# Kernel tuning notes

Hardware: AMD Instinct MI355X
Metric: run time of the kernel (lower is better)

The kernel has to match this reference:

```python
import jax, jax.numpy as jnp
import numpy as np
import math

B, N, ND, ED, CD, H = 4, 128, 256, 128, 256, 8
D = ND // H

def _ln(x):
    m = jnp.mean(x, axis=-1, keepdims=True)
    v = jnp.mean((x - m) ** 2, axis=-1, keepdims=True)
    return (x - m) / jnp.sqrt(v + 1e-5)

def _lrelu(x):
    return jax.nn.leaky_relu(x, negative_slope=0.1)

def setup_inputs() -> dict:
    key = jax.random.key(0)
    ks = jax.random.split(key, 16)
    rn = lambda k, s: jax.random.normal(k, s, jnp.float32) * 0.02
    return {
        "nodes": jax.random.normal(ks[0], (B, N, ND), jnp.float32),
        "edges": jax.random.normal(ks[1], (B, N, N, ED), jnp.float32),
        "conds": jax.random.normal(ks[2], (B, 1, CD), jnp.float32),
        "Wc": rn(ks[3], (CD, 4 * ND)), "bc": jnp.zeros((4 * ND,), jnp.float32),
        "Wqkv": rn(ks[4], (ND, 3 * ND)), "bqkv": jnp.zeros((3 * ND,), jnp.float32),
        "Wss": rn(ks[5], (ED, 2 * ND)), "bss": jnp.zeros((2 * ND,), jnp.float32),
        "Wno": rn(ks[6], (ND, ND)), "bno": jnp.zeros((ND,), jnp.float32),
        "Weo": rn(ks[7], (ND, ED)), "beo": jnp.zeros((ED,), jnp.float32),
        "Wn1": rn(ks[8], (ND, 4 * ND)), "bn1": jnp.zeros((4 * ND,), jnp.float32),
        "Wn2": rn(ks[9], (4 * ND, ND)), "bn2": jnp.zeros((ND,), jnp.float32),
        "We1": rn(ks[10], (ED, ED)), "be1": jnp.zeros((ED,), jnp.float32),
        "We2": rn(ks[11], (ED, ED)), "be2": jnp.zeros((ED,), jnp.float32),
    }

def reference(nodes, edges, conds, Wc, bc, Wqkv, bqkv, Wss, bss, Wno, bno, Weo, beo, Wn1, bn1, Wn2, bn2, We1, be1, We2, be2):
    b, n, _ = nodes.shape
    # FiLM conditioning (4 chunks, torch chunk order)
    cond = conds @ Wc + bc  # (b,1,4*ND)
    mul_in, add_in, mul_out, add_out = jnp.split(cond, 4, axis=-1)
    n_in = _lrelu(_ln(nodes) * (1.0 + mul_in) + add_in)
    e_in = _lrelu(_ln(edges))
    # attention
    qkv = n_in @ Wqkv + bqkv
    q, k, v = jnp.split(qkv, 3, axis=-1)
    q = q.reshape(b, n, H, D).transpose(0, 2, 1, 3)  # (b,h,n,d)
    k = k.reshape(b, n, H, D).transpose(0, 2, 1, 3)
    v = v.reshape(b, n, H, D).transpose(0, 2, 1, 3)
    # outer-product attention tensor (b,h,q,k,d)
    attn5 = q[:, :, :, None, :] * k[:, :, None, :, :]
    ss = e_in @ Wss + bss  # (b,n,n,2*ND)
    shift, scale = jnp.split(ss, 2, axis=-1)
    shift = shift.reshape(b, n, n, H, D).transpose(0, 3, 1, 2, 4)
    scale = scale.reshape(b, n, n, H, D).transpose(0, 3, 1, 2, 4)
    new_e = attn5 * scale + attn5 + shift  # (b,h,q,k,d)
    logits = jnp.sum(new_e, axis=4) / math.sqrt(D)  # (b,h,q,k)
    attn = jax.nn.softmax(logits, axis=2)  # softmax over dim=2 as in source
    # weighted values -> (b,n,H*D), matching values.view/transpose/flatten layout
    wv = jnp.einsum('bhqk,bhkd->bqhd', attn, v).reshape(b, n, ND)
    new_edges = new_e.transpose(0, 2, 3, 1, 4).reshape(b, n, n, ND)
    delta_nodes = wv @ Wno + bno
    delta_edges = _lrelu(new_edges) @ Weo + beo
    nodes = nodes + delta_nodes
    edges = edges + delta_edges
    # FiLM-normed MLP blocks
    n_out = _lrelu(_ln(nodes) * (1.0 + mul_out) + add_out)
    nodes = nodes + (_lrelu(n_out @ Wn1 + bn1) @ Wn2 + bn2)
    e_out = _lrelu(_ln(edges))
    edges = edges + (_lrelu(e_out @ We1 + be1) @ We2 + be2)
    return (nodes, edges)
```

## Files before the change

### kernel.cpp

```cpp
#include <hip/hip_runtime.h>
#include <hip/hip_bf16.h>

#define BB 4
#define NN 128
#define NH 8

typedef __attribute__((ext_vector_type(8))) short short8;
typedef __attribute__((ext_vector_type(4))) float f32x4;

__device__ __forceinline__ float lrelu(float x){ return fmaxf(x, 0.1f*x); }
__device__ __forceinline__ unsigned short f2b(float x){
  __hip_bfloat16 h = __float2bfloat16(x);
  return *reinterpret_cast<unsigned short*>(&h);
}
__device__ __forceinline__ short8 ldf(const unsigned short* p){ return *(const short8*)p; }


__global__ __launch_bounds__(256) void k_setup(
    const float* Wss, const float* Weo, const float* We1, const float* We2,
    const float* Wqkv, const float* Wno, const float* Wn1, const float* Wn2,
    const float* conds, const float* Wc, const float* bc,
    unsigned short* wbf, float* cond){
  __shared__ float tile[32][33];
  __shared__ float c[256];
  int bid = blockIdx.x, t = threadIdx.x;
  if (bid < 896){
    const float* src; int K, N; size_t doff; int tid;
    if      (bid < 64)  { src=Wss;  K=128;  N=512;  doff=0;      tid=bid; }
    else if (bid < 96)  { src=Weo;  K=256;  N=128;  doff=65536;  tid=bid-64; }
    else if (bid < 112) { src=We1;  K=128;  N=128;  doff=98304;  tid=bid-96; }
    else if (bid < 128) { src=We2;  K=128;  N=128;  doff=114688; tid=bid-112; }
    else if (bid < 320) { src=Wqkv; K=256;  N=768;  doff=131072; tid=bid-128; }
    else if (bid < 384) { src=Wno;  K=256;  N=256;  doff=327680; tid=bid-320; }
    else if (bid < 640) { src=Wn1;  K=256;  N=1024; doff=393216; tid=bid-384; }
    else                { src=Wn2;  K=1024; N=256;  doff=655360; tid=bid-640; }
    int ntk = K >> 5;
    int k0 = (tid % ntk) * 32, n0 = (tid / ntk) * 32;
    int r = t >> 3, c4 = (t & 7) * 4;
    float4 v = *(const float4*)(src + (size_t)(k0+r)*N + n0 + c4);
    tile[r][c4+0]=v.x; tile[r][c4+1]=v.y; tile[r][c4+2]=v.z; tile[r][c4+3]=v.w;
    __syncthreads();
    ushort4 o;
    o.x = f2b(tile[c4+0][r]); o.y = f2b(tile[c4+1][r]);
    o.z = f2b(tile[c4+2][r]); o.w = f2b(tile[c4+3][r]);
    *(ushort4*)(wbf + doff + (size_t)(n0+r)*K + k0 + c4) = o;
  } else {
    int i = bid - 896;
    int b = i >> 2, j = (i&3)*256 + t;
    c[t] = conds[(size_t)b*256 + t];
    __syncthreads();
    float acc = bc[j];
    for (int kk = 0; kk < 256; kk++) acc += c[kk]*Wc[(size_t)kk*1024 + j];
    cond[b*1024 + j] = acc;
  }
}

#define NSTR 260
__global__ __launch_bounds__(256) void k_nodeA(const float* __restrict__ nodes,
    const float* __restrict__ cond, const unsigned short* __restrict__ WqkvT,
    const float* __restrict__ bqkv, float* __restrict__ qbuf,
    float* __restrict__ kT, unsigned short* __restrict__ vT){
  __shared__ float nbuf[16*NSTR];
  __shared__ __align__(16) unsigned short abuf[16*272];
  __shared__ float psum[256], psq[256], mrow[16], irow[16];
  int t = threadIdx.x;
  int rg = blockIdx.x >> 2, slice = blockIdx.x & 3;
  int b = rg >> 3, n0 = (rg & 7)*16;
  int l = t & 63, w = t >> 6, l15 = l & 15, q = l >> 4;

  const float4* src = (const float4*)(nodes + ((size_t)(b*128+n0))*256);
  #pragma unroll
  for (int i = 0; i < 4; i++){
    int f = t + i*256; int r = f >> 6, c4 = f & 63;
    *(float4*)(nbuf + r*NSTR + c4*4) = src[f];
  }
  __syncthreads();
  {
    int r = t >> 4, p = t & 15;
    float s = 0.f, s2 = 0.f;
    #pragma unroll
    for (int i = 0; i < 16; i++){ float v = nbuf[r*NSTR + p + 16*i]; s += v; s2 += v*v; }
    psum[t] = s; psq[t] = s2;
  }
  __syncthreads();
  if (t < 16){
    float s = 0.f, s2 = 0.f;
    #pragma unroll
    for (int i = 0; i < 16; i++){ s += psum[t*16+i]; s2 += psq[t*16+i]; }
    float m = s*(1.f/256);
    mrow[t] = m; irow[t] = rsqrtf(s2*(1.f/256) - m*m + 1e-5f);
  }
  __syncthreads();
  #pragma unroll
  for (int i = 0; i < 16; i++){
    int f = t + i*256; int r = f >> 8, cc = f & 255;
    float x = (nbuf[r*NSTR+cc]-mrow[r])*irow[r]*(1.f+cond[b*1024+cc]) + cond[b*1024+256+cc];
    abuf[r*272+cc] = f2b(lrelu(x));
  }
  __syncthreads();
  short8 af[8];
  #pragma unroll
  for (int k = 0; k < 8; k++) af[k] = ldf(abuf + l15*272 + k*32 + q*8);
  #pragma unroll
  for (int tt = 0; tt < 3; tt++){
    int cc = slice*192 + w*48 + tt*16 + l15;
    const unsigned short* bp = WqkvT + (size_t)cc*256 + q*8;
    f32x4 acc = {0.f,0.f,0.f,0.f};
    #pragma unroll
    for (int k = 0; k < 8; k++) acc = __builtin_amdgcn_mfma_f32_16x16x32_bf16(af[k], ldf(bp + k*32), acc,0,0,0);
    float bb = bqkv[cc];
    if (cc < 256){
      #pragma unroll
      for (int r = 0; r < 4; r++) qbuf[(size_t)(b*128+n0+q*4+r)*256 + cc] = acc[r] + bb;
    } else if (cc < 512){
      float4 kv; kv.x = acc[0]+bb; kv.y = acc[1]+bb; kv.z = acc[2]+bb; kv.w = acc[3]+bb;
      *(float4*)(kT + ((size_t)(b*256 + cc-256))*128 + n0 + q*4) = kv;
    } else {
      ushort4 vv; vv.x = f2b(acc[0]+bb); vv.y = f2b(acc[1]+bb); vv.z = f2b(acc[2]+bb); vv.w = f2b(acc[3]+bb);
      *(ushort4*)(vT + ((size_t)(b*256 + cc-512))*128 + n0 + q*4) = vv;
    }
  }
}

#define ASTR 144
#define LSTR 272
__global__ __launch_bounds__(256) void k_edge(
    const float* __restrict__ edges, const float* __restrict__ qbuf, const float* __restrict__ kT,
    const unsigned short* __restrict__ WssT, const float* __restrict__ bss,
    const unsigned short* __restrict__ WeoT, const float* __restrict__ beo,
    const unsigned short* __restrict__ We1T, const float* __restrict__ be1,
    const unsigned short* __restrict__ We2T, const float* __restrict__ be2,
    float* __restrict__ logitsT, float* __restrict__ out_edges){
  __shared__ __align__(16) unsigned short abuf[32*ASTR];
  __shared__ __align__(16) unsigned short lbuf[32*LSTR];
  __shared__ float qvs[256];
  __shared__ float redS[32][4], redQ[32][4], mrow[32], irow[32];

  int t = threadIdx.x;
  int p0 = blockIdx.x * 32;
  int b  = p0 >> 14, qi = (p0 >> 7) & 127, ki0 = p0 & 127;
  int w = t >> 6, l15 = t & 15, q = (t & 63) >> 4;

  {
    qvs[t] = qbuf[(size_t)(b*128 + qi)*256 + t];
    const float4* src = (const float4*)(edges + (size_t)p0*128);
    #pragma unroll
    for (int i=0;i<4;i++){
      int idx = t + i*256;
      float4 ev = src[idx];
      int r = idx >> 5, c4 = idx & 31;
      float s  = ev.x + ev.y + ev.z + ev.w;
      float s2 = ev.x*ev.x + ev.y*ev.y + ev.z*ev.z + ev.w*ev.w;
      #pragma unroll
      for (int mm=1; mm<32; mm<<=1){ s += __shfl_xor(s,mm); s2 += __shfl_xor(s2,mm); }
      float m = s*(1.f/128);
      float inv = rsqrtf(s2*(1.f/128) - m*m + 1e-5f);
      ushort4 pk;
      pk.x = f2b(lrelu((ev.x - m)*inv)); pk.y = f2b(lrelu((ev.y - m)*inv));
      pk.z = f2b(lrelu((ev.z - m)*inv)); pk.w = f2b(lrelu((ev.w - m)*inv));
      *(ushort4*)(abuf + r*ASTR + c4*4) = pk;
    }
  }
  __syncthreads();

  const float isd = 0.17677669529663687f;
  {
    short8 af[2][4];
    #pragma unroll
    for (int s=0;s<2;s++)
      #pragma unroll
      for (int k=0;k<4;k++) af[s][k] = ldf(abuf + (s*16+l15)*ASTR + k*32 + q*8);
    #pragma unroll
    for (int h2=0; h2<2; h2++){
      int h = w*2 + h2;
      float ps[2][4] = {{0.f,0.f,0.f,0.f},{0.f,0.f,0.f,0.f}};
      #pragma unroll
      for (int tt=0; tt<2; tt++){
        int cc = h*32 + tt*16 + l15;
        const unsigned short* bsp = WssT + (size_t)cc*128 + q*8;
        const unsigned short* bcp = WssT + (size_t)(cc+256)*128 + q*8;
        f32x4 aS[2], aC[2];
        aS[0]={0.f,0.f,0.f,0.f}; aS[1]=aS[0]; aC[0]=aS[0]; aC[1]=aS[0];
        #pragma unroll
        for (int k=0;k<4;k++){
          short8 b0 = ldf(bsp + k*32);
          short8 b1 = ldf(bcp + k*32);
          aS[0] = __builtin_amdgcn_mfma_f32_16x16x32_bf16(af[0][k], b0, aS[0],0,0,0);
          aS[1] = __builtin_amdgcn_mfma_f32_16x16x32_bf16(af[1][k], b0, aS[1],0,0,0);
          aC[0] = __builtin_amdgcn_mfma_f32_16x16x32_bf16(af[0][k], b1, aC[0],0,0,0);
          aC[1] = __builtin_amdgcn_mfma_f32_16x16x32_bf16(af[1][k], b1, aC[1],0,0,0);
        }
        float bS = bss[cc], bC = bss[256+cc], qv = qvs[cc];
        #pragma unroll
        for (int s=0;s<2;s++){
          float4 kv4 = *(const float4*)(kT + ((size_t)(b*256+cc))*128 + ki0 + s*16 + q*4);
          float kvv[4] = {kv4.x, kv4.y, kv4.z, kv4.w};
          #pragma unroll
          for (int r=0;r<4;r++){
            int row = s*16 + q*4 + r;
            float ne = qv*kvv[r]*(1.f + aC[s][r] + bC) + aS[s][r] + bS;
            lbuf[row*LSTR + cc] = f2b(lrelu(ne));
            ps[s][r] += ne;
          }
        }
      }
      #pragma unroll
      for (int s=0;s<2;s++)
        #pragma unroll
        for (int r=0;r<4;r++){
          float v = ps[s][r];
          v += __shfl_xor(v,1); v += __shfl_xor(v,2);
          v += __shfl_xor(v,4); v += __shfl_xor(v,8);
          if (l15 == 0){
            int ki = ki0 + s*16 + q*4 + r;
            logitsT[((size_t)(b*8+h)*128 + ki)*128 + qi] = v * isd;
          }
        }
    }
  }
  __syncthreads();

  float res[2][2][4];
  {
    f32x4 acc[2][2];
    acc[0][0]={0.f,0.f,0.f,0.f}; acc[0][1]=acc[0][0]; acc[1][0]=acc[0][0]; acc[1][1]=acc[0][0];
    #pragma unroll
    for (int k=0;k<8;k++){
      short8 lf0 = ldf(lbuf + l15*LSTR + k*32 + q*8);
      short8 lf1 = ldf(lbuf + (16+l15)*LSTR + k*32 + q*8);
      #pragma unroll
      for (int tt=0;tt<2;tt++){
        int ec = w*32 + tt*16 + l15;
        short8 bf = ldf(WeoT + (size_t)ec*256 + k*32 + q*8);
        acc[tt][0] = __builtin_amdgcn_mfma_f32_16x16x32_bf16(lf0, bf, acc[tt][0],0,0,0);
        acc[tt][1] = __builtin_amdgcn_mfma_f32_16x16x32_bf16(lf1, bf, acc[tt][1],0,0,0);
      }
    }
    #pragma unroll
    for (int tt=0;tt<2;tt++){
      int ec = w*32 + tt*16 + l15;
      float bb = beo[ec];
      #pragma unroll
      for (int s=0;s<2;s++)
        #pragma unroll
        for (int r=0;r<4;r++){
          int row = s*16 + q*4 + r;
          res[tt][s][r] = edges[(size_t)(p0+row)*128 + ec] + acc[tt][s][r] + bb;
        }
    }
  }
  #pragma unroll
  for (int s=0;s<2;s++)
    #pragma unroll
    for (int r=0;r<4;r++){
      float ps = res[0][s][r] + res[1][s][r];
      float p2 = res[0][s][r]*res[0][s][r] + res[1][s][r]*res[1][s][r];
      ps += __shfl_xor(ps,1); ps += __shfl_xor(ps,2); ps += __shfl_xor(ps,4); ps += __shfl_xor(ps,8);
      p2 += __shfl_xor(p2,1); p2 += __shfl_xor(p2,2); p2 += __shfl_xor(p2,4); p2 += __shfl_xor(p2,8);
      if (l15 == 0){ redS[s*16+q*4+r][w] = ps; redQ[s*16+q*4+r][w] = p2; }
    }
  __syncthreads();
  if (t < 32){
    float s = redS[t][0]+redS[t][1]+redS[t][2]+redS[t][3];
    float s2 = redQ[t][0]+redQ[t][1]+redQ[t][2]+redQ[t][3];
    float m = s*(1.f/128);
    mrow[t] = m; irow[t] = rsqrtf(s2*(1.f/128) - m*m + 1e-5f);
  }
  __syncthreads();
  #pragma unroll
  for (int tt=0;tt<2;tt++){
    int ec = w*32 + tt*16 + l15;
    #pragma unroll
    for (int s=0;s<2;s++)
      #pragma unroll
      for (int r=0;r<4;r++){
        int row = s*16 + q*4 + r;
        abuf[row*ASTR + ec] = f2b(lrelu((res[tt][s][r] - mrow[row])*irow[row]));
      }
  }
  __syncthreads();

  unsigned short* hbuf = lbuf;
  {
    f32x4 acc[2][2];
    acc[0][0]={0.f,0.f,0.f,0.f}; acc[0][1]=acc[0][0]; acc[1][0]=acc[0][0]; acc[1][1]=acc[0][0];
    #pragma unroll
    for (int k=0;k<4;k++){
      short8 a0 = ldf(abuf + l15*ASTR + k*32 + q*8);
      short8 a1 = ldf(abuf + (16+l15)*ASTR + k*32 + q*8);
      #pragma unroll
      for (int tt=0;tt<2;tt++){
        int ec = w*32 + tt*16 + l15;
        short8 bf = ldf(We1T + (size_t)ec*128 + k*32 + q*8);
        acc[tt][0] = __builtin_amdgcn_mfma_f32_16x16x32_bf16(a0, bf, acc[tt][0],0,0,0);
        acc[tt][1] = __builtin_amdgcn_mfma_f32_16x16x32_bf16(a1, bf, acc[tt][1],0,0,0);
      }
    }
    #pragma unroll
    for (int tt=0;tt<2;tt++){
      int ec = w*32 + tt*16 + l15;
      float bb = be1[ec];
      #pragma unroll
      for (int r=0;r<4;r++){
        hbuf[(q*4+r)*ASTR + ec] = f2b(lrelu(acc[tt][0][r] + bb));
        hbuf[(16+q*4+r)*ASTR + ec] = f2b(lrelu(acc[tt][1][r] + bb));
      }
    }
  }
  __syncthreads();
  {
    f32x4 acc[2][2];
    acc[0][0]={0.f,0.f,0.f,0.f}; acc[0][1]=acc[0][0]; acc[1][0]=acc[0][0]; acc[1][1]=acc[0][0];
    #pragma unroll
    for (int k=0;k<4;k++){
      short8 h0 = ldf(hbuf + l15*ASTR + k*32 + q*8);
      short8 h1 = ldf(hbuf + (16+l15)*ASTR + k*32 + q*8);
      #pragma unroll
      for (int tt=0;tt<2;tt++){
        int ec = w*32 + tt*16 + l15;
        short8 bf = ldf(We2T + (size_t)ec*128 + k*32 + q*8);
        acc[tt][0] = __builtin_amdgcn_mfma_f32_16x16x32_bf16(h0, bf, acc[tt][0],0,0,0);
        acc[tt][1] = __builtin_amdgcn_mfma_f32_16x16x32_bf16(h1, bf, acc[tt][1],0,0,0);
      }
    }
    #pragma unroll
    for (int tt=0;tt<2;tt++){
      int ec = w*32 + tt*16 + l15;
      float bb = be2[ec];
      #pragma unroll
      for (int r=0;r<4;r++){
        out_edges[(size_t)(p0 + q*4+r)*128 + ec] = res[tt][0][r] + acc[tt][0][r] + bb;
        out_edges[(size_t)(p0 + 16 + q*4+r)*128 + ec] = res[tt][1][r] + acc[tt][1][r] + bb;
      }
    }
  }
}

__global__ __launch_bounds__(256) void k_attn(const float* __restrict__ logitsT,
                                              unsigned short* __restrict__ attnB){
  __shared__ float tile[32][129];
  __shared__ float mS[128], sS[128];
  int t = threadIdx.x, w = t >> 6, l = t & 63;
  const float* base = logitsT + (size_t)blockIdx.x * 16384;
  for (int i = 0; i < 32; i++){
    int ki = w*32 + i;
    float x0 = base[ki*128 + l], x1 = base[ki*128 + 64 + l];
    float mx = fmaxf(x0, x1);
    #pragma unroll
    for (int m=1;m<64;m<<=1) mx = fmaxf(mx, __shfl_xor(mx,m));
    float s = __expf(x0-mx) + __expf(x1-mx);
    #pragma unroll
    for (int m=1;m<64;m<<=1) s += __shfl_xor(s,m);
    if (l == 0){ mS[ki] = mx; sS[ki] = 1.f/s; }
  }
  __syncthreads();
  unsigned short* obase = attnB + (size_t)blockIdx.x * 16384;
  for (int c = 0; c < 4; c++){
    int q0 = c*32;
    #pragma unroll
    for (int i = 0; i < 16; i++){
      int idx = t + i*256; int ki = idx >> 5, qq = idx & 31;
      tile[qq][ki] = base[ki*128 + q0 + qq];
    }
    __syncthreads();
    #pragma unroll
    for (int i = 0; i < 16; i++){
      int idx = t + i*256; int qq = idx >> 7, ki = idx & 127;
      obase[(q0+qq)*128 + ki] = f2b(__expf(tile[qq][ki] - mS[ki]) * sS[ki]);
    }
    __syncthreads();
  }
}

#define AB 272
__global__ __launch_bounds__(256) void k_nodeB(
    const unsigned short* __restrict__ attnB, const unsigned short* __restrict__ vT,
    const float* __restrict__ nodes, const float* __restrict__ cond,
    const unsigned short* __restrict__ WnoT, const float* __restrict__ bno,
    const unsigned short* __restrict__ Wn1T, const float* __restrict__ bn1,
    float* __restrict__ nodes1ws, unsigned short* __restrict__ hiddenB){
  __shared__ __align__(16) unsigned short abuf[16*AB];
  __shared__ float redS[16][4], redQ[16][4], mrow[16], irow[16];
  int t = threadIdx.x;
  int rg = blockIdx.x >> 2, slice = blockIdx.x & 3;
  int b = rg >> 3, n0 = (rg & 7)*16;
  int w = t >> 6, l15 = t & 15, q = (t & 63) >> 4;

  #pragma unroll
  for (int h2=0; h2<2; h2++){
    int h = w*2 + h2;
    const unsigned short* ap = attnB + ((size_t)(b*8+h)*128 + n0 + l15)*128 + q*8;
    short8 af[4];
    #pragma unroll
    for (int k=0;k<4;k++) af[k] = ldf(ap + k*32);
    #pragma unroll
    for (int tt=0;tt<2;tt++){
      int cc = h*32 + tt*16 + l15;
      const unsigned short* bp = vT + (size_t)(b*256+cc)*128 + q*8;
      f32x4 acc = {0.f,0.f,0.f,0.f};
      #pragma unroll
      for (int k=0;k<4;k++) acc = __builtin_amdgcn_mfma_f32_16x16x32_bf16(af[k], ldf(bp + k*32), acc,0,0,0);
      #pragma unroll
      for (int r=0;r<4;r++) abuf[(q*4+r)*AB + cc] = f2b(acc[r]);
    }
  }
  __syncthreads();

  float res[4][4];
  {
    short8 aw[8];
    #pragma unroll
    for (int k=0;k<8;k++) aw[k] = ldf(abuf + l15*AB + k*32 + q*8);
    #pragma unroll
    for (int tt=0;tt<4;tt++){
      int cc = w*64 + tt*16 + l15;
      const unsigned short* bp = WnoT + (size_t)cc*256 + q*8;
      f32x4 acc = {0.f,0.f,0.f,0.f};
      #pragma unroll
      for (int k=0;k<8;k++) acc = __builtin_amdgcn_mfma_f32_16x16x32_bf16(aw[k], ldf(bp + k*32), acc,0,0,0);
      float bb = bno[cc];
      #pragma unroll
      for (int r=0;r<4;r++)
        res[tt][r] = nodes[(size_t)(b*128+n0+q*4+r)*256 + cc] + acc[r] + bb;
    }
  }
  #pragma unroll
  for (int r=0;r<4;r++){
    float ps = res[0][r]+res[1][r]+res[2][r]+res[3][r];
    float p2 = res[0][r]*res[0][r]+res[1][r]*res[1][r]+res[2][r]*res[2][r]+res[3][r]*res[3][r];
    ps += __shfl_xor(ps,1); ps += __shfl_xor(ps,2); ps += __shfl_xor(ps,4); ps += __shfl_xor(ps,8);
    p2 += __shfl_xor(p2,1); p2 += __shfl_xor(p2,2); p2 += __shfl_xor(p2,4); p2 += __shfl_xor(p2,8);
    if (l15 == 0){ redS[q*4+r][w] = ps; redQ[q*4+r][w] = p2; }
  }
  __syncthreads();
  if (t < 16){
    float s = redS[t][0]+redS[t][1]+redS[t][2]+redS[t][3];
    float s2 = redQ[t][0]+redQ[t][1]+redQ[t][2]+redQ[t][3];
    float m = s*(1.f/256);
    mrow[t] = m; irow[t] = rsqrtf(s2*(1.f/256) - m*m + 1e-5f);
  }
  __syncthreads();
  #pragma unroll
  for (int tt=0;tt<4;tt++){
    int cc = w*64 + tt*16 + l15;
    float mul = 1.f + cond[b*1024 + 512 + cc];
    float add = cond[b*1024 + 768 + cc];
    #pragma unroll
    for (int r=0;r<4;r++){
      int row = q*4+r;
      abuf[row*AB + cc] = f2b(lrelu((res[tt][r] - mrow[row])*irow[row]*mul + add));
    }
  }
  if (slice == 0){
    #pragma unroll
    for (int tt=0;tt<4;tt++){
      int cc = w*64 + tt*16 + l15;
      #pragma unroll
      for (int r=0;r<4;r++)
        nodes1ws[(size_t)(rg*16 + q*4+r)*256 + cc] = res[tt][r];
    }
  }
  __syncthreads();
  {
    short8 a2[8];
    #pragma unroll
    for (int k=0;k<8;k++) a2[k] = ldf(abuf + l15*AB + k*32 + q*8);
    #pragma unroll
    for (int tt=0;tt<4;tt++){
      int cc = slice*256 + w*64 + tt*16 + l15;
      const unsigned short* bp = Wn1T + (size_t)cc*256 + q*8;
      f32x4 acc = {0.f,0.f,0.f,0.f};
      #pragma unroll
      for (int k=0;k<8;k++) acc = __builtin_amdgcn_mfma_f32_16x16x32_bf16(a2[k], ldf(bp + k*32), acc,0,0,0);
      float bb = bn1[cc];
      #pragma unroll
      for (int r=0;r<4;r++)
        hiddenB[((size_t)rg*16 + q*4+r)*1024 + cc] = f2b(lrelu(acc[r] + bb));
    }
  }
}

__global__ __launch_bounds__(256) void k_nodeC(
    const unsigned short* __restrict__ hiddenB, const float* __restrict__ nodes1ws,
    const unsigned short* __restrict__ Wn2T, const float* __restrict__ bn2,
    float* __restrict__ out_nodes){
  int t = threadIdx.x;
  int rg = blockIdx.x >> 2, cs = blockIdx.x & 3;
  int w = t >> 6, l15 = t & 15, q = (t & 63) >> 4;
  int cc = cs*64 + w*16 + l15;
  const unsigned short* ap = hiddenB + ((size_t)rg*16 + l15)*1024 + q*8;
  const unsigned short* bp = Wn2T + (size_t)cc*1024 + q*8;
  f32x4 acc = {0.f,0.f,0.f,0.f};
  #pragma unroll
  for (int k=0;k<32;k++)
    acc = __builtin_amdgcn_mfma_f32_16x16x32_bf16(ldf(ap + k*32), ldf(bp + k*32), acc,0,0,0);
  float bb = bn2[cc];
  #pragma unroll
  for (int r=0;r<4;r++){
    size_t row = (size_t)rg*16 + q*4 + r;
    out_nodes[row*256 + cc] = nodes1ws[row*256 + cc] + acc[r] + bb;
  }
}

extern "C" void kernel_launch(void* const* d_in, const int* in_sizes, int n_inp,
                              void* d_out, int out_size, void* d_ws, size_t ws_size,
                              hipStream_t stream){
  const float* nodes = (const float*)d_in[0];
  const float* edges = (const float*)d_in[1];
  const float* conds = (const float*)d_in[2];
  const float* Wc   = (const float*)d_in[3];
  const float* bc   = (const float*)d_in[4];
  const float* Wqkv = (const float*)d_in[5];
  const float* bqkv = (const float*)d_in[6];
  const float* Wss  = (const float*)d_in[7];
  const float* bss  = (const float*)d_in[8];
  const float* Wno  = (const float*)d_in[9];
  const float* bno  = (const float*)d_in[10];
  const float* Weo  = (const float*)d_in[11];
  const float* beo  = (const float*)d_in[12];
  const float* Wn1  = (const float*)d_in[13];
  const float* bn1  = (const float*)d_in[14];
  const float* Wn2  = (const float*)d_in[15];
  const float* bn2  = (const float*)d_in[16];
  const float* We1  = (const float*)d_in[17];
  const float* be1  = (const float*)d_in[18];
  const float* We2  = (const float*)d_in[19];
  const float* be2  = (const float*)d_in[20];

  float* ws       = (float*)d_ws;
  float* cond     = ws;
  float* qbuf     = cond + 4096;
  float* kT       = qbuf + 131072;
  float* logitsT  = kT + 131072;
  float* nodes1ws = logitsT + 524288;
  unsigned short* attnB   = (unsigned short*)(nodes1ws + 131072);
  unsigned short* vT      = attnB + 524288;
  unsigned short* hiddenB = vT + 131072;
  unsigned short* wbf     = hiddenB + 524288;

  unsigned short* WssT  = wbf;
  unsigned short* WeoT  = wbf + 65536;
  unsigned short* We1T  = wbf + 98304;
  unsigned short* We2T  = wbf + 114688;
  unsigned short* WqkvT = wbf + 131072;
  unsigned short* WnoT  = wbf + 327680;
  unsigned short* Wn1T  = wbf + 393216;
  unsigned short* Wn2T  = wbf + 655360;

  float* out_nodes = (float*)d_out;
  float* out_edges = out_nodes + 131072;

  k_setup<<<912, 256, 0, stream>>>(Wss, Weo, We1, We2, Wqkv, Wno, Wn1, Wn2,
                                   conds, Wc, bc, wbf, cond);
  k_nodeA<<<128, 256, 0, stream>>>(nodes, cond, WqkvT, bqkv, qbuf, kT, vT);
  k_edge<<<BB*NN*NN/32, 256, 0, stream>>>(edges, qbuf, kT, WssT, bss, WeoT, beo,
                                          We1T, be1, We2T, be2, logitsT, out_edges);
  k_attn<<<BB*NH, 256, 0, stream>>>(logitsT, attnB);
  k_nodeB<<<128, 256, 0, stream>>>(attnB, vT, nodes, cond, WnoT, bno, Wn1T, bn1,
                                   nodes1ws, hiddenB);
  k_nodeC<<<128, 256, 0, stream>>>(hiddenB, nodes1ws, Wn2T, bn2, out_nodes);
}
```

Measured before the change: 257.3 us.

## Double edge tile rows per block and split softmax kernel across more blocks

The edge kernel now handles 64 edge rows per block instead of 32. Each weight fragment loaded from global memory therefore feeds four MFMA row tiles instead of two, which halves weight reloads per edge, and the LDS row stride is changed. Separately, the attention softmax kernel is split into 8 slices per batch-head (256 blocks instead of 32), so it fills more compute units. The cost is higher register and LDS pressure in the edge kernel and only half as many edge blocks, which may reduce occupancy.

```diff
diff --git a/kernel.cpp b/kernel.cpp
--- a/kernel.cpp
+++ b/kernel.cpp
@@ -123,7 +123,7 @@
 }
 
 #define ASTR 144
-#define LSTR 272
+#define LSTR 264
 __global__ __launch_bounds__(256) void k_edge(
     const float* __restrict__ edges, const float* __restrict__ qbuf, const float* __restrict__ kT,
     const unsigned short* __restrict__ WssT, const float* __restrict__ bss,
@@ -131,13 +131,13 @@
     const unsigned short* __restrict__ We1T, const float* __restrict__ be1,
     const unsigned short* __restrict__ We2T, const float* __restrict__ be2,
     float* __restrict__ logitsT, float* __restrict__ out_edges){
-  __shared__ __align__(16) unsigned short abuf[32*ASTR];
-  __shared__ __align__(16) unsigned short lbuf[32*LSTR];
+  __shared__ __align__(16) unsigned short abuf[64*ASTR];
+  __shared__ __align__(16) unsigned short lbuf[64*LSTR];
   __shared__ float qvs[256];
-  __shared__ float redS[32][4], redQ[32][4], mrow[32], irow[32];
+  __shared__ float redS[64][4], redQ[64][4], mrow[64], irow[64];
 
   int t = threadIdx.x;
-  int p0 = blockIdx.x * 32;
+  int p0 = blockIdx.x * 64;
   int b  = p0 >> 14, qi = (p0 >> 7) & 127, ki0 = p0 & 127;
   int w = t >> 6, l15 = t & 15, q = (t & 63) >> 4;
 
@@ -145,7 +145,7 @@
     qvs[t] = qbuf[(size_t)(b*128 + qi)*256 + t];
     const float4* src = (const float4*)(edges + (size_t)p0*128);
     #pragma unroll
-    for (int i=0;i<4;i++){
+    for (int i=0;i<8;i++){
       int idx = t + i*256;
       float4 ev = src[idx];
       int r = idx >> 5, c4 = idx & 31;
@@ -165,34 +165,36 @@
 
   const float isd = 0.17677669529663687f;
   {
-    short8 af[2][4];
-    #pragma unroll
-    for (int s=0;s<2;s++)
+    short8 af[4][4];
+    #pragma unroll
+    for (int s=0;s<4;s++)
       #pragma unroll
       for (int k=0;k<4;k++) af[s][k] = ldf(abuf + (s*16+l15)*ASTR + k*32 + q*8);
     #pragma unroll
     for (int h2=0; h2<2; h2++){
       int h = w*2 + h2;
-      float ps[2][4] = {{0.f,0.f,0.f,0.f},{0.f,0.f,0.f,0.f}};
+      float ps[4][4] = {{0,0,0,0},{0,0,0,0},{0,0,0,0},{0,0,0,0}};
       #pragma unroll
       for (int tt=0; tt<2; tt++){
         int cc = h*32 + tt*16 + l15;
         const unsigned short* bsp = WssT + (size_t)cc*128 + q*8;
         const unsigned short* bcp = WssT + (size_t)(cc+256)*128 + q*8;
-        f32x4 aS[2], aC[2];
-        aS[0]={0.f,0.f,0.f,0.f}; aS[1]=aS[0]; aC[0]=aS[0]; aC[1]=aS[0];
+        f32x4 aS[4], aC[4];
+        #pragma unroll
+        for (int s=0;s<4;s++){ aS[s]={0.f,0.f,0.f,0.f}; aC[s]={0.f,0.f,0.f,0.f}; }
         #pragma unroll
         for (int k=0;k<4;k++){
           short8 b0 = ldf(bsp + k*32);
           short8 b1 = ldf(bcp + k*32);
-          aS[0] = __builtin_amdgcn_mfma_f32_16x16x32_bf16(af[0][k], b0, aS[0],0,0,0);
-          aS[1] = __builtin_amdgcn_mfma_f32_16x16x32_bf16(af[1][k], b0, aS[1],0,0,0);
-          aC[0] = __builtin_amdgcn_mfma_f32_16x16x32_bf16(af[0][k], b1, aC[0],0,0,0);
-          aC[1] = __builtin_amdgcn_mfma_f32_16x16x32_bf16(af[1][k], b1, aC[1],0,0,0);
+          #pragma unroll
+          for (int s=0;s<4;s++){
+            aS[s] = __builtin_amdgcn_mfma_f32_16x16x32_bf16(af[s][k], b0, aS[s],0,0,0);
+            aC[s] = __builtin_amdgcn_mfma_f32_16x16x32_bf16(af[s][k], b1, aC[s],0,0,0);
+          }
         }
         float bS = bss[cc], bC = bss[256+cc], qv = qvs[cc];
         #pragma unroll
-        for (int s=0;s<2;s++){
+        for (int s=0;s<4;s++){
           float4 kv4 = *(const float4*)(kT + ((size_t)(b*256+cc))*128 + ki0 + s*16 + q*4);
           float kvv[4] = {kv4.x, kv4.y, kv4.z, kv4.w};
           #pragma unroll
@@ -205,7 +207,7 @@
         }
       }
       #pragma unroll
-      for (int s=0;s<2;s++)
+      for (int s=0;s<4;s++)
         #pragma unroll
         for (int r=0;r<4;r++){
           float v = ps[s][r];
@@ -220,20 +222,25 @@
   }
   __syncthreads();
 
-  float res[2][2][4];
-  {
-    f32x4 acc[2][2];
-    acc[0][0]={0.f,0.f,0.f,0.f}; acc[0][1]=acc[0][0]; acc[1][0]=acc[0][0]; acc[1][1]=acc[0][0];
+  float res[2][4][4];
+  {
+    f32x4 acc[2][4];
+    #pragma unroll
+    for (int tt=0;tt<2;tt++)
+      #pragma unroll
+      for (int s=0;s<4;s++) acc[tt][s] = {0.f,0.f,0.f,0.f};
     #pragma unroll
     for (int k=0;k<8;k++){
-      short8 lf0 = ldf(lbuf + l15*LSTR + k*32 + q*8);
-      short8 lf1 = ldf(lbuf + (16+l15)*LSTR + k*32 + q*8);
+      short8 lf[4];
+      #pragma unroll
+      for (int s=0;s<4;s++) lf[s] = ldf(lbuf + (s*16+l15)*LSTR + k*32 + q*8);
       #pragma unroll
       for (int tt=0;tt<2;tt++){
         int ec = w*32 + tt*16 + l15;
         short8 bf = ldf(WeoT + (size_t)ec*256 + k*32 + q*8);
-        acc[tt][0] = __builtin_amdgcn_mfma_f32_16x16x32_bf16(lf0, bf, acc[tt][0],0,0,0);
-        acc[tt][1] = __builtin_amdgcn_mfma_f32_16x16x32_bf16(lf1, bf, acc[tt][1],0,0,0);
+        #pragma unroll
+        for (int s=0;s<4;s++)
+          acc[tt][s] = __builtin_amdgcn_mfma_f32_16x16x32_bf16(lf[s], bf, acc[tt][s],0,0,0);
       }
     }
     #pragma unroll
@@ -241,7 +248,7 @@
       int ec = w*32 + tt*16 + l15;
       float bb = beo[ec];
       #pragma unroll
-      for (int s=0;s<2;s++)
+      for (int s=0;s<4;s++)
         #pragma unroll
         for (int r=0;r<4;r++){
           int row = s*16 + q*4 + r;
@@ -250,7 +257,7 @@
     }
   }
   #pragma unroll
-  for (int s=0;s<2;s++)
+  for (int s=0;s<4;s++)
     #pragma unroll
     for (int r=0;r<4;r++){
       float ps = res[0][s][r] + res[1][s][r];
@@ -260,7 +267,7 @@
       if (l15 == 0){ redS[s*16+q*4+r][w] = ps; redQ[s*16+q*4+r][w] = p2; }
     }
   __syncthreads();
-  if (t < 32){
+  if (t < 64){
     float s = redS[t][0]+redS[t][1]+redS[t][2]+redS[t][3];
     float s2 = redQ[t][0]+redQ[t][1]+redQ[t][2]+redQ[t][3];
     float m = s*(1.f/128);
@@ -271,7 +278,7 @@
   for (int tt=0;tt<2;tt++){
     int ec = w*32 + tt*16 + l15;
     #pragma unroll
-    for (int s=0;s<2;s++)
+    for (int s=0;s<4;s++)
       #pragma unroll
       for (int r=0;r<4;r++){
         int row = s*16 + q*4 + r;
@@ -282,18 +289,23 @@
 
   unsigned short* hbuf = lbuf;
   {
-    f32x4 acc[2][2];
-    acc[0][0]={0.f,0.f,0.f,0.f}; acc[0][1]=acc[0][0]; acc[1][0]=acc[0][0]; acc[1][1]=acc[0][0];
+    f32x4 acc[2][4];
+    #pragma unroll
+    for (int tt=0;tt<2;tt++)
+      #pragma unroll
+      for (int s=0;s<4;s++) acc[tt][s] = {0.f,0.f,0.f,0.f};
     #pragma unroll
     for (int k=0;k<4;k++){
-      short8 a0 = ldf(abuf + l15*ASTR + k*32 + q*8);
-      short8 a1 = ldf(abuf + (16+l15)*ASTR + k*32 + q*8);
+      short8 af2[4];
+      #pragma unroll
+      for (int s=0;s<4;s++) af2[s] = ldf(abuf + (s*16+l15)*ASTR + k*32 + q*8);
       #pragma unroll
       for (int tt=0;tt<2;tt++){
         int ec = w*32 + tt*16 + l15;
         short8 bf = ldf(We1T + (size_t)ec*128 + k*32 + q*8);
-        acc[tt][0] = __builtin_amdgcn_mfma_f32_16x16x32_bf16(a0, bf, acc[tt][0],0,0,0);
-        acc[tt][1] = __builtin_amdgcn_mfma_f32_16x16x32_bf16(a1, bf, acc[tt][1],0,0,0);
+        #pragma unroll
+        for (int s=0;s<4;s++)
+          acc[tt][s] = __builtin_amdgcn_mfma_f32_16x16x32_bf16(af2[s], bf, acc[tt][s],0,0,0);
       }
     }
     #pragma unroll
@@ -301,26 +313,31 @@
       int ec = w*32 + tt*16 + l15;
       float bb = be1[ec];
       #pragma unroll
-      for (int r=0;r<4;r++){
-        hbuf[(q*4+r)*ASTR + ec] = f2b(lrelu(acc[tt][0][r] + bb));
-        hbuf[(16+q*4+r)*ASTR + ec] = f2b(lrelu(acc[tt][1][r] + bb));
-      }
-    }
-  }
-  __syncthreads();
-  {
-    f32x4 acc[2][2];
-    acc[0][0]={0.f,0.f,0.f,0.f}; acc[0][1]=acc[0][0]; acc[1][0]=acc[0][0]; acc[1][1]=acc[0][0];
+      for (int s=0;s<4;s++)
+        #pragma unroll
+        for (int r=0;r<4;r++)
+          hbuf[(s*16+q*4+r)*ASTR + ec] = f2b(lrelu(acc[tt][s][r] + bb));
+    }
+  }
+  __syncthreads();
+  {
+    f32x4 acc[2][4];
+    #pragma unroll
+    for (int tt=0;tt<2;tt++)
+      #pragma unroll
+      for (int s=0;s<4;s++) acc[tt][s] = {0.f,0.f,0.f,0.f};
     #pragma unroll
     for (int k=0;k<4;k++){
-      short8 h0 = ldf(hbuf + l15*ASTR + k*32 + q*8);
-      short8 h1 = ldf(hbuf + (16+l15)*ASTR + k*32 + q*8);
+      short8 hf[4];
+      #pragma unroll
+      for (int s=0;s<4;s++) hf[s] = ldf(hbuf + (s*16+l15)*ASTR + k*32 + q*8);
       #pragma unroll
       for (int tt=0;tt<2;tt++){
         int ec = w*32 + tt*16 + l15;
         short8 bf = ldf(We2T + (size_t)ec*128 + k*32 + q*8);
-        acc[tt][0] = __builtin_amdgcn_mfma_f32_16x16x32_bf16(h0, bf, acc[tt][0],0,0,0);
-        acc[tt][1] = __builtin_amdgcn_mfma_f32_16x16x32_bf16(h1, bf, acc[tt][1],0,0,0);
+        #pragma unroll
+        for (int s=0;s<4;s++)
+          acc[tt][s] = __builtin_amdgcn_mfma_f32_16x16x32_bf16(hf[s], bf, acc[tt][s],0,0,0);
       }
     }
     #pragma unroll
@@ -328,23 +345,33 @@
       int ec = w*32 + tt*16 + l15;
       float bb = be2[ec];
       #pragma unroll
-      for (int r=0;r<4;r++){
-        out_edges[(size_t)(p0 + q*4+r)*128 + ec] = res[tt][0][r] + acc[tt][0][r] + bb;
-        out_edges[(size_t)(p0 + 16 + q*4+r)*128 + ec] = res[tt][1][r] + acc[tt][1][r] + bb;
-      }
+      for (int s=0;s<4;s++)
+        #pragma unroll
+        for (int r=0;r<4;r++){
+          int row = s*16 + q*4 + r;
+          out_edges[(size_t)(p0+row)*128 + ec] = res[tt][s][r] + acc[tt][s][r] + bb;
+        }
     }
   }
 }
 
 __global__ __launch_bounds__(256) void k_attn(const float* __restrict__ logitsT,
                                               unsigned short* __restrict__ attnB){
-  __shared__ float tile[32][129];
-  __shared__ float mS[128], sS[128];
+  __shared__ float tile[16][132];
+  __shared__ float mS[16], sS[16];
+  int bh = blockIdx.x >> 3, slice = blockIdx.x & 7;
   int t = threadIdx.x, w = t >> 6, l = t & 63;
-  const float* base = logitsT + (size_t)blockIdx.x * 16384;
-  for (int i = 0; i < 32; i++){
-    int ki = w*32 + i;
-    float x0 = base[ki*128 + l], x1 = base[ki*128 + 64 + l];
+  const float* base = logitsT + (size_t)bh*16384 + slice*16*128;
+  #pragma unroll
+  for (int i = 0; i < 8; i++){
+    int idx = t + i*256; int ki = idx >> 7, qq = idx & 127;
+    tile[ki][qq] = base[ki*128 + qq];
+  }
+  __syncthreads();
+  #pragma unroll
+  for (int i = 0; i < 4; i++){
+    int ki = w*4 + i;
+    float x0 = tile[ki][l], x1 = tile[ki][l+64];
     float mx = fmaxf(x0, x1);
     #pragma unroll
     for (int m=1;m<64;m<<=1) mx = fmaxf(mx, __shfl_xor(mx,m));
@@ -354,21 +381,11 @@
     if (l == 0){ mS[ki] = mx; sS[ki] = 1.f/s; }
   }
   __syncthreads();
-  unsigned short* obase = attnB + (size_t)blockIdx.x * 16384;
-  for (int c = 0; c < 4; c++){
-    int q0 = c*32;
-    #pragma unroll
-    for (int i = 0; i < 16; i++){
-      int idx = t + i*256; int ki = idx >> 5, qq = idx & 31;
-      tile[qq][ki] = base[ki*128 + q0 + qq];
-    }
-    __syncthreads();
-    #pragma unroll
-    for (int i = 0; i < 16; i++){
-      int idx = t + i*256; int qq = idx >> 7, ki = idx & 127;
-      obase[(q0+qq)*128 + ki] = f2b(__expf(tile[qq][ki] - mS[ki]) * sS[ki]);
-    }
-    __syncthreads();
+  unsigned short* obase = attnB + (size_t)bh*16384 + slice*16;
+  #pragma unroll
+  for (int i = 0; i < 8; i++){
+    int idx = t + i*256; int qq = idx >> 4, kk = idx & 15;
+    obase[qq*128 + kk] = f2b(__expf(tile[kk][qq] - mS[kk]) * sS[kk]);
   }
 }
 
@@ -553,9 +570,9 @@
   k_setup<<<912, 256, 0, stream>>>(Wss, Weo, We1, We2, Wqkv, Wno, Wn1, Wn2,
                                    conds, Wc, bc, wbf, cond);
   k_nodeA<<<128, 256, 0, stream>>>(nodes, cond, WqkvT, bqkv, qbuf, kT, vT);
-  k_edge<<<BB*NN*NN/32, 256, 0, stream>>>(edges, qbuf, kT, WssT, bss, WeoT, beo,
+  k_edge<<<BB*NN*NN/64, 256, 0, stream>>>(edges, qbuf, kT, WssT, bss, WeoT, beo,
                                           We1T, be1, We2T, be2, logitsT, out_edges);
-  k_attn<<<BB*NH, 256, 0, stream>>>(logitsT, attnB);
+  k_attn<<<BB*NH*8, 256, 0, stream>>>(logitsT, attnB);
   k_nodeB<<<128, 256, 0, stream>>>(attnB, vT, nodes, cond, WnoT, bno, Wn1T, bn1,
                                    nodes1ws, hiddenB);
   k_nodeC<<<128, 256, 0, stream>>>(hiddenB, nodes1ws, Wn2T, bn2, out_nodes);
```

After: 218.7 us. 15.0% less time.
